# Kernel tuning notes

Hardware: AMD Instinct MI355X
Metric: run time of the kernel (lower is better)

The kernel has to match this reference:

```python
import jax, jax.numpy as jnp
import numpy as np

N = 1 << 20          # ray samples
POS_DIM = 32         # levels * feature_dim (hash_encoding is identity stub)
DENSITY_W = 64
COLOR_W = 64


def sh4_encoding(d):
    # Fourth-order (degree-4, 16-component) real spherical harmonics, vectorized.
    x, y, z = d[..., 0], d[..., 1], d[..., 2]
    xx, yy, zz = x * x, y * y, z * z
    c0 = jnp.full_like(x, 0.28209479177387814)
    comps = [
        c0,
        0.4886025119029199 * y,
        0.4886025119029199 * z,
        0.4886025119029199 * x,
        1.0925484305920792 * x * y,
        1.0925484305920792 * y * z,
        0.9461746957575601 * zz - 0.31539156525252,
        1.0925484305920792 * x * z,
        0.5462742152960396 * (xx - yy),
        0.5900435899266435 * y * (3 * xx - yy),
        2.890611442640554 * x * y * z,
        0.4570457994644658 * y * (5 * zz - 1),
        0.3731763325901154 * z * (5 * zz - 3),
        0.4570457994644658 * x * (5 * zz - 1),
        1.445305721320277 * z * (xx - yy),
        0.5900435899266435 * x * (xx - 3 * yy),
    ]
    return jnp.stack(comps, axis=-1)  # [..., 16]


def setup_inputs() -> dict:
    key = jax.random.key(0)
    ks = jax.random.split(key, 8)
    def dense_init(k, fan_in, fan_out):
        # flax default: lecun_normal kernel, zeros bias
        w = jax.random.normal(k, (fan_in, fan_out), dtype=jnp.float32) / np.sqrt(fan_in)
        b = jnp.zeros((fan_out,), dtype=jnp.float32)
        return w, b
    position = jax.random.normal(ks[0], (N, POS_DIM), dtype=jnp.float32)
    direction = jax.random.normal(ks[1], (N, 3), dtype=jnp.float32)
    W1, b1 = dense_init(ks[2], POS_DIM, DENSITY_W)
    W2, b2 = dense_init(ks[3], DENSITY_W, 16)
    W3, b3 = dense_init(ks[4], 16 + 16, COLOR_W)
    W4, b4 = dense_init(ks[5], COLOR_W, COLOR_W)
    W5, b5 = dense_init(ks[6], COLOR_W, 3)
    return {
        "position": position, "direction": direction,
        "W1": W1, "b1": b1, "W2": W2, "b2": b2,
        "W3": W3, "b3": b3, "W4": W4, "b4": b4,
        "W5": W5, "b5": b5,
    }


def reference(position, direction, W1, b1, W2, b2, W3, b3, W4, b4, W5, b5):
    # Density MLP
    h = jax.nn.relu(position @ W1 + b1)        # [N, 64]
    density = h @ W2 + b2                      # [N, 16]
    # Color MLP on concat(density_feat, SH(dir))
    enc_dir = sh4_encoding(direction)          # [N, 16]
    c = jnp.concatenate([density, enc_dir], axis=-1)  # [N, 32]
    c = jax.nn.relu(c @ W3 + b3)               # [N, 64]
    c = jax.nn.relu(c @ W4 + b4)               # [N, 64]
    c = c @ W5 + b5                            # [N, 3]
    color = jax.nn.sigmoid(c)                  # high_dynamic_range=False
    return (density, color)
```

## Files before the change

### kernel.cpp

```cpp
#include <hip/hip_runtime.h>
#include <hip/hip_bf16.h>

typedef __bf16 bf16_t;
typedef __bf16 bf16x8 __attribute__((ext_vector_type(8)));
typedef float  f32x4  __attribute__((ext_vector_type(4)));

#define TPW   8
#define WAVES 4
#define ROWS_PER_BLOCK (WAVES * TPW * 16)
#define HSTRIDE 65
#define CSTRIDE 33

__device__ __forceinline__ bf16x8 ldrow8(const float* base, size_t elem_off) {
    const float* p = base + elem_off;
    f32x4 a = *(const f32x4*)p;
    f32x4 b = *(const f32x4*)(p + 4);
    bf16x8 r;
    #pragma unroll
    for (int j = 0; j < 4; ++j) { r[j] = (bf16_t)a[j]; r[j+4] = (bf16_t)b[j]; }
    return r;
}

__global__ __launch_bounds__(256) void nerf_fused(
    const float* __restrict__ pos, const float* __restrict__ dir,
    const float* __restrict__ W1, const float* __restrict__ b1,
    const float* __restrict__ W2, const float* __restrict__ b2,
    const float* __restrict__ W3, const float* __restrict__ b3,
    const float* __restrict__ W4, const float* __restrict__ b4,
    const float* __restrict__ W5, const float* __restrict__ b5,
    float* __restrict__ outD, float* __restrict__ outC)
{
    __shared__ float hbuf[WAVES][16 * HSTRIDE];
    __shared__ float cbuf[WAVES][16 * CSTRIDE];

    const int tid  = threadIdx.x;
    const int w    = tid >> 6;
    const int lane = tid & 63;
    const int q    = lane >> 4;
    const int n    = lane & 15;

    float* hb = hbuf[w];
    float* cb = cbuf[w];

    bf16x8 w1f[4], w2f[2], w3f[4], w4f[2][4], w5f[2];
    #pragma unroll
    for (int t = 0; t < 4; ++t)
        #pragma unroll
        for (int j = 0; j < 8; ++j)
            w1f[t][j] = (bf16_t)W1[(8*q + j) * 64 + 16*t + n];
    #pragma unroll
    for (int kt = 0; kt < 2; ++kt)
        #pragma unroll
        for (int j = 0; j < 8; ++j)
            w2f[kt][j] = (bf16_t)W2[(32*kt + 8*q + j) * 16 + n];
    #pragma unroll
    for (int t = 0; t < 4; ++t)
        #pragma unroll
        for (int j = 0; j < 8; ++j)
            w3f[t][j] = (bf16_t)W3[(8*q + j) * 64 + 16*t + n];
    #pragma unroll
    for (int kt = 0; kt < 2; ++kt)
        #pragma unroll
        for (int t = 0; t < 4; ++t)
            #pragma unroll
            for (int j = 0; j < 8; ++j)
                w4f[kt][t][j] = (bf16_t)W4[(32*kt + 8*q + j) * 64 + 16*t + n];
    #pragma unroll
    for (int kt = 0; kt < 2; ++kt)
        #pragma unroll
        for (int j = 0; j < 8; ++j)
            w5f[kt][j] = (n < 3) ? (bf16_t)W5[(32*kt + 8*q + j) * 3 + n]
                                 : (bf16_t)0.0f;
    float b1f[4], b3f[4], b4f[4];
    #pragma unroll
    for (int t = 0; t < 4; ++t) {
        b1f[t] = b1[16*t + n];
        b3f[t] = b3[16*t + n];
        b4f[t] = b4[16*t + n];
    }
    const float b2f = b2[n];
    const float b5f = (n < 3) ? b5[n] : 0.0f;

    const f32x4 zero4 = {0.f, 0.f, 0.f, 0.f};

    const int waveRow0 = blockIdx.x * ROWS_PER_BLOCK + w * (TPW * 16);

    bf16x8 pfrag = ldrow8(pos, (size_t)(waveRow0 + n) * 32 + 8*q);

    for (int t = 0; t < TPW; ++t) {
        const int row0 = waveRow0 + t * 16;
        const int tn   = (t + 1 < TPW) ? t + 1 : t;
        bf16x8 pnext = ldrow8(pos, (size_t)(waveRow0 + tn*16 + n) * 32 + 8*q);

        const size_t db = (size_t)(row0 + n) * 3;
        const float dx = dir[db + 0];
        const float dy = dir[db + 1];
        const float dz = dir[db + 2];

        f32x4 acc1[4];
        #pragma unroll
        for (int tt = 0; tt < 4; ++tt)
            acc1[tt] = __builtin_amdgcn_mfma_f32_16x16x32_bf16(pfrag, w1f[tt], zero4, 0, 0, 0);
        #pragma unroll
        for (int tt = 0; tt < 4; ++tt)
            #pragma unroll
            for (int r = 0; r < 4; ++r)
                hb[(4*q + r) * HSTRIDE + 16*tt + n] = fmaxf(acc1[tt][r] + b1f[tt], 0.f);
        __syncthreads();
        bf16x8 a2[2];
        #pragma unroll
        for (int kt = 0; kt < 2; ++kt)
            #pragma unroll
            for (int j = 0; j < 8; ++j)
                a2[kt][j] = (bf16_t)hb[n * HSTRIDE + 32*kt + 8*q + j];

        f32x4 acc2 = __builtin_amdgcn_mfma_f32_16x16x32_bf16(a2[0], w2f[0], zero4, 0, 0, 0);
        acc2 = __builtin_amdgcn_mfma_f32_16x16x32_bf16(a2[1], w2f[1], acc2, 0, 0, 0);
        #pragma unroll
        for (int r = 0; r < 4; ++r)
            cb[(4*q + r) * CSTRIDE + n] = acc2[r] + b2f;

        {
            const float xx = dx*dx, yy = dy*dy, zz = dz*dz;
            float c0, c1, c2, c3;
            if (q == 0) {
                c0 = 0.28209479177387814f;
                c1 = 0.4886025119029199f * dy;
                c2 = 0.4886025119029199f * dz;
                c3 = 0.4886025119029199f * dx;
            } else if (q == 1) {
                c0 = 1.0925484305920792f * dx * dy;
                c1 = 1.0925484305920792f * dy * dz;
                c2 = 0.9461746957575601f * zz - 0.31539156525252f;
                c3 = 1.0925484305920792f * dx * dz;
            } else if (q == 2) {
                c0 = 0.5462742152960396f * (xx - yy);
                c1 = 0.5900435899266435f * dy * (3.f*xx - yy);
                c2 = 2.890611442640554f * dx * dy * dz;
                c3 = 0.4570457994644658f * dy * (5.f*zz - 1.f);
            } else {
                c0 = 0.3731763325901154f * dz * (5.f*zz - 3.f);
                c1 = 0.4570457994644658f * dx * (5.f*zz - 1.f);
                c2 = 1.445305721320277f  * dz * (xx - yy);
                c3 = 0.5900435899266435f * dx * (xx - 3.f*yy);
            }
            float* p = cb + n * CSTRIDE + 16 + 4*q;
            p[0] = c0; p[1] = c1; p[2] = c2; p[3] = c3;
        }
        __syncthreads();

        {
            const int rr = lane >> 2;
            const int cg = lane & 3;
            const float* src = cb + rr * CSTRIDE + 4*cg;
            f32x4 dv = { src[0], src[1], src[2], src[3] };
            *(f32x4*)(outD + (size_t)(row0 + rr) * 16 + 4*cg) = dv;
        }

        bf16x8 a3;
        #pragma unroll
        for (int j = 0; j < 8; ++j)
            a3[j] = (bf16_t)cb[n * CSTRIDE + 8*q + j];
        f32x4 acc3[4];
        #pragma unroll
        for (int tt = 0; tt < 4; ++tt)
            acc3[tt] = __builtin_amdgcn_mfma_f32_16x16x32_bf16(a3, w3f[tt], zero4, 0, 0, 0);
        __syncthreads();
        #pragma unroll
        for (int tt = 0; tt < 4; ++tt)
            #pragma unroll
            for (int r = 0; r < 4; ++r)
                hb[(4*q + r) * HSTRIDE + 16*tt + n] = fmaxf(acc3[tt][r] + b3f[tt], 0.f);
        __syncthreads();
        bf16x8 a4[2];
        #pragma unroll
        for (int kt = 0; kt < 2; ++kt)
            #pragma unroll
            for (int j = 0; j < 8; ++j)
                a4[kt][j] = (bf16_t)hb[n * HSTRIDE + 32*kt + 8*q + j];

        f32x4 acc4[4];
        #pragma unroll
        for (int tt = 0; tt < 4; ++tt) {
            acc4[tt] = __builtin_amdgcn_mfma_f32_16x16x32_bf16(a4[0], w4f[0][tt], zero4, 0, 0, 0);
            acc4[tt] = __builtin_amdgcn_mfma_f32_16x16x32_bf16(a4[1], w4f[1][tt], acc4[tt], 0, 0, 0);
        }
        __syncthreads();
        #pragma unroll
        for (int tt = 0; tt < 4; ++tt)
            #pragma unroll
            for (int r = 0; r < 4; ++r)
                hb[(4*q + r) * HSTRIDE + 16*tt + n] = fmaxf(acc4[tt][r] + b4f[tt], 0.f);
        __syncthreads();
        bf16x8 a5[2];
        #pragma unroll
        for (int kt = 0; kt < 2; ++kt)
            #pragma unroll
            for (int j = 0; j < 8; ++j)
                a5[kt][j] = (bf16_t)hb[n * HSTRIDE + 32*kt + 8*q + j];

        f32x4 acc5 = __builtin_amdgcn_mfma_f32_16x16x32_bf16(a5[0], w5f[0], zero4, 0, 0, 0);
        acc5 = __builtin_amdgcn_mfma_f32_16x16x32_bf16(a5[1], w5f[1], acc5, 0, 0, 0);
        if (n < 3) {
            #pragma unroll
            for (int r = 0; r < 4; ++r) {
                float v = acc5[r] + b5f;
                outC[(size_t)(row0 + 4*q + r) * 3 + n] = 1.f / (1.f + __expf(-v));
            }
        }
        __syncthreads();

        pfrag = pnext;
    }
}

extern "C" void kernel_launch(void* const* d_in, const int* in_sizes, int n_in,
                              void* d_out, int out_size, void* d_ws, size_t ws_size,
                              hipStream_t stream) {
    const float* pos = (const float*)d_in[0];
    const float* dir = (const float*)d_in[1];
    const float* W1  = (const float*)d_in[2];
    const float* b1  = (const float*)d_in[3];
    const float* W2  = (const float*)d_in[4];
    const float* b2  = (const float*)d_in[5];
    const float* W3  = (const float*)d_in[6];
    const float* b3  = (const float*)d_in[7];
    const float* W4  = (const float*)d_in[8];
    const float* b4  = (const float*)d_in[9];
    const float* W5  = (const float*)d_in[10];
    const float* b5  = (const float*)d_in[11];

    const int N = in_sizes[0] / 32;
    float* outD = (float*)d_out;
    float* outC = outD + (size_t)N * 16;

    const int grid = N / ROWS_PER_BLOCK;
    nerf_fused<<<grid, WAVES * 64, 0, stream>>>(pos, dir, W1, b1, W2, b2, W3, b3,
                                                W4, b4, W5, b5, outD, outC);
}
```

Before: 287.4 us.

## Replace block barriers with wave-local fences, vectorize LDS access, compute SH in registers

Each wave only touches its own LDS slice, so the block-wide __syncthreads calls are replaced with compiler memory fences and rely on in-wave lockstep execution. LDS strides are padded to 68/36 so rows can be read as aligned float4 vectors. The SH direction encoding is now computed straight into the MFMA A-fragment registers for the upper lane groups instead of going through LDS. Color output is staged through LDS so one store per lane replaces the strided per-lane writes. The main risk is correctness: the compiler-only fences do not emit LDS waitcnt and depend on wave-synchronous behaviour, and the padded strides may cause bank conflicts.

```diff
diff --git a/kernel.cpp b/kernel.cpp
--- a/kernel.cpp
+++ b/kernel.cpp
@@ -8,8 +8,10 @@
 #define TPW   8
 #define WAVES 4
 #define ROWS_PER_BLOCK (WAVES * TPW * 16)
-#define HSTRIDE 65
-#define CSTRIDE 33
+#define HS 68
+#define CS 36
+
+#define FENCE() __asm__ volatile("" ::: "memory")
 
 __device__ __forceinline__ bf16x8 ldrow8(const float* base, size_t elem_off) {
     const float* p = base + elem_off;
@@ -30,8 +32,8 @@
     const float* __restrict__ W5, const float* __restrict__ b5,
     float* __restrict__ outD, float* __restrict__ outC)
 {
-    __shared__ float hbuf[WAVES][16 * HSTRIDE];
-    __shared__ float cbuf[WAVES][16 * CSTRIDE];
+    __shared__ float hbuf[WAVES][16 * HS];
+    __shared__ float cbuf[WAVES][16 * CS];
 
     const int tid  = threadIdx.x;
     const int w    = tid >> 6;
@@ -92,92 +94,103 @@
         const int tn   = (t + 1 < TPW) ? t + 1 : t;
         bf16x8 pnext = ldrow8(pos, (size_t)(waveRow0 + tn*16 + n) * 32 + 8*q);
 
-        const size_t db = (size_t)(row0 + n) * 3;
-        const float dx = dir[db + 0];
-        const float dy = dir[db + 1];
-        const float dz = dir[db + 2];
-
         f32x4 acc1[4];
         #pragma unroll
         for (int tt = 0; tt < 4; ++tt)
             acc1[tt] = __builtin_amdgcn_mfma_f32_16x16x32_bf16(pfrag, w1f[tt], zero4, 0, 0, 0);
         #pragma unroll
-        for (int tt = 0; tt < 4; ++tt)
-            #pragma unroll
-            for (int r = 0; r < 4; ++r)
-                hb[(4*q + r) * HSTRIDE + 16*tt + n] = fmaxf(acc1[tt][r] + b1f[tt], 0.f);
-        __syncthreads();
+        for (int r = 0; r < 4; ++r) {
+            float* p = hb + (4*q + r) * HS + n;
+            p[0]  = fmaxf(acc1[0][r] + b1f[0], 0.f);
+            p[16] = fmaxf(acc1[1][r] + b1f[1], 0.f);
+            p[32] = fmaxf(acc1[2][r] + b1f[2], 0.f);
+            p[48] = fmaxf(acc1[3][r] + b1f[3], 0.f);
+        }
+        FENCE();
         bf16x8 a2[2];
         #pragma unroll
-        for (int kt = 0; kt < 2; ++kt)
-            #pragma unroll
-            for (int j = 0; j < 8; ++j)
-                a2[kt][j] = (bf16_t)hb[n * HSTRIDE + 32*kt + 8*q + j];
+        for (int kt = 0; kt < 2; ++kt) {
+            const f32x4* pr = (const f32x4*)(hb + n * HS + 32*kt + 8*q);
+            f32x4 u0 = pr[0], u1 = pr[1];
+            #pragma unroll
+            for (int j = 0; j < 4; ++j) { a2[kt][j] = (bf16_t)u0[j]; a2[kt][4+j] = (bf16_t)u1[j]; }
+        }
 
         f32x4 acc2 = __builtin_amdgcn_mfma_f32_16x16x32_bf16(a2[0], w2f[0], zero4, 0, 0, 0);
         acc2 = __builtin_amdgcn_mfma_f32_16x16x32_bf16(a2[1], w2f[1], acc2, 0, 0, 0);
-        #pragma unroll
-        for (int r = 0; r < 4; ++r)
-            cb[(4*q + r) * CSTRIDE + n] = acc2[r] + b2f;
-
         {
-            const float xx = dx*dx, yy = dy*dy, zz = dz*dz;
-            float c0, c1, c2, c3;
-            if (q == 0) {
-                c0 = 0.28209479177387814f;
-                c1 = 0.4886025119029199f * dy;
-                c2 = 0.4886025119029199f * dz;
-                c3 = 0.4886025119029199f * dx;
-            } else if (q == 1) {
-                c0 = 1.0925484305920792f * dx * dy;
-                c1 = 1.0925484305920792f * dy * dz;
-                c2 = 0.9461746957575601f * zz - 0.31539156525252f;
-                c3 = 1.0925484305920792f * dx * dz;
-            } else if (q == 2) {
-                c0 = 0.5462742152960396f * (xx - yy);
-                c1 = 0.5900435899266435f * dy * (3.f*xx - yy);
-                c2 = 2.890611442640554f * dx * dy * dz;
-                c3 = 0.4570457994644658f * dy * (5.f*zz - 1.f);
-            } else {
-                c0 = 0.3731763325901154f * dz * (5.f*zz - 3.f);
-                c1 = 0.4570457994644658f * dx * (5.f*zz - 1.f);
-                c2 = 1.445305721320277f  * dz * (xx - yy);
-                c3 = 0.5900435899266435f * dx * (xx - 3.f*yy);
-            }
-            float* p = cb + n * CSTRIDE + 16 + 4*q;
-            p[0] = c0; p[1] = c1; p[2] = c2; p[3] = c3;
-        }
-        __syncthreads();
+            float* p = cb + (4*q) * CS + n;
+            p[0]    = acc2[0] + b2f;
+            p[CS]   = acc2[1] + b2f;
+            p[2*CS] = acc2[2] + b2f;
+            p[3*CS] = acc2[3] + b2f;
+        }
+        FENCE();
 
         {
             const int rr = lane >> 2;
             const int cg = lane & 3;
-            const float* src = cb + rr * CSTRIDE + 4*cg;
-            f32x4 dv = { src[0], src[1], src[2], src[3] };
+            f32x4 dv = *(const f32x4*)(cb + rr * CS + 4*cg);
             *(f32x4*)(outD + (size_t)(row0 + rr) * 16 + 4*cg) = dv;
         }
 
+        float av[8];
+        {
+            const f32x4* pr = (const f32x4*)(cb + n * CS + 8*(q & 1));
+            f32x4 u0 = pr[0], u1 = pr[1];
+            #pragma unroll
+            for (int j = 0; j < 4; ++j) { av[j] = u0[j]; av[4+j] = u1[j]; }
+        }
+        if (q >= 2) {
+            const size_t db = (size_t)(row0 + n) * 3;
+            const float x = dir[db + 0], y = dir[db + 1], z = dir[db + 2];
+            const float xx = x*x, yy = y*y, zz = z*z;
+            if (q == 2) {
+                av[0] = 0.28209479177387814f;
+                av[1] = 0.4886025119029199f * y;
+                av[2] = 0.4886025119029199f * z;
+                av[3] = 0.4886025119029199f * x;
+                av[4] = 1.0925484305920792f * x * y;
+                av[5] = 1.0925484305920792f * y * z;
+                av[6] = 0.9461746957575601f * zz - 0.31539156525252f;
+                av[7] = 1.0925484305920792f * x * z;
+            } else {
+                av[0] = 0.5462742152960396f * (xx - yy);
+                av[1] = 0.5900435899266435f * y * (3.f*xx - yy);
+                av[2] = 2.890611442640554f * x * y * z;
+                av[3] = 0.4570457994644658f * y * (5.f*zz - 1.f);
+                av[4] = 0.3731763325901154f * z * (5.f*zz - 3.f);
+                av[5] = 0.4570457994644658f * x * (5.f*zz - 1.f);
+                av[6] = 1.445305721320277f  * z * (xx - yy);
+                av[7] = 0.5900435899266435f * x * (xx - 3.f*yy);
+            }
+        }
         bf16x8 a3;
         #pragma unroll
-        for (int j = 0; j < 8; ++j)
-            a3[j] = (bf16_t)cb[n * CSTRIDE + 8*q + j];
+        for (int j = 0; j < 8; ++j) a3[j] = (bf16_t)av[j];
+
         f32x4 acc3[4];
         #pragma unroll
         for (int tt = 0; tt < 4; ++tt)
             acc3[tt] = __builtin_amdgcn_mfma_f32_16x16x32_bf16(a3, w3f[tt], zero4, 0, 0, 0);
-        __syncthreads();
-        #pragma unroll
-        for (int tt = 0; tt < 4; ++tt)
-            #pragma unroll
-            for (int r = 0; r < 4; ++r)
-                hb[(4*q + r) * HSTRIDE + 16*tt + n] = fmaxf(acc3[tt][r] + b3f[tt], 0.f);
-        __syncthreads();
+        FENCE();
+        #pragma unroll
+        for (int r = 0; r < 4; ++r) {
+            float* p = hb + (4*q + r) * HS + n;
+            p[0]  = fmaxf(acc3[0][r] + b3f[0], 0.f);
+            p[16] = fmaxf(acc3[1][r] + b3f[1], 0.f);
+            p[32] = fmaxf(acc3[2][r] + b3f[2], 0.f);
+            p[48] = fmaxf(acc3[3][r] + b3f[3], 0.f);
+        }
+        FENCE();
         bf16x8 a4[2];
         #pragma unroll
-        for (int kt = 0; kt < 2; ++kt)
-            #pragma unroll
-            for (int j = 0; j < 8; ++j)
-                a4[kt][j] = (bf16_t)hb[n * HSTRIDE + 32*kt + 8*q + j];
+        for (int kt = 0; kt < 2; ++kt) {
+            const f32x4* pr = (const f32x4*)(hb + n * HS + 32*kt + 8*q);
+            f32x4 u0 = pr[0], u1 = pr[1];
+            #pragma unroll
+            for (int j = 0; j < 4; ++j) { a4[kt][j] = (bf16_t)u0[j]; a4[kt][4+j] = (bf16_t)u1[j]; }
+        }
 
         f32x4 acc4[4];
         #pragma unroll
@@ -185,30 +198,41 @@
             acc4[tt] = __builtin_amdgcn_mfma_f32_16x16x32_bf16(a4[0], w4f[0][tt], zero4, 0, 0, 0);
             acc4[tt] = __builtin_amdgcn_mfma_f32_16x16x32_bf16(a4[1], w4f[1][tt], acc4[tt], 0, 0, 0);
         }
-        __syncthreads();
-        #pragma unroll
-        for (int tt = 0; tt < 4; ++tt)
-            #pragma unroll
-            for (int r = 0; r < 4; ++r)
-                hb[(4*q + r) * HSTRIDE + 16*tt + n] = fmaxf(acc4[tt][r] + b4f[tt], 0.f);
-        __syncthreads();
+        FENCE();
+        #pragma unroll
+        for (int r = 0; r < 4; ++r) {
+            float* p = hb + (4*q + r) * HS + n;
+            p[0]  = fmaxf(acc4[0][r] + b4f[0], 0.f);
+            p[16] = fmaxf(acc4[1][r] + b4f[1], 0.f);
+            p[32] = fmaxf(acc4[2][r] + b4f[2], 0.f);
+            p[48] = fmaxf(acc4[3][r] + b4f[3], 0.f);
+        }
+        FENCE();
         bf16x8 a5[2];
         #pragma unroll
-        for (int kt = 0; kt < 2; ++kt)
-            #pragma unroll
-            for (int j = 0; j < 8; ++j)
-                a5[kt][j] = (bf16_t)hb[n * HSTRIDE + 32*kt + 8*q + j];
+        for (int kt = 0; kt < 2; ++kt) {
+            const f32x4* pr = (const f32x4*)(hb + n * HS + 32*kt + 8*q);
+            f32x4 u0 = pr[0], u1 = pr[1];
+            #pragma unroll
+            for (int j = 0; j < 4; ++j) { a5[kt][j] = (bf16_t)u0[j]; a5[kt][4+j] = (bf16_t)u1[j]; }
+        }
 
         f32x4 acc5 = __builtin_amdgcn_mfma_f32_16x16x32_bf16(a5[0], w5f[0], zero4, 0, 0, 0);
         acc5 = __builtin_amdgcn_mfma_f32_16x16x32_bf16(a5[1], w5f[1], acc5, 0, 0, 0);
         if (n < 3) {
+            float* p = cb + (4*q) * CS + 32 + n;
             #pragma unroll
             for (int r = 0; r < 4; ++r) {
                 float v = acc5[r] + b5f;
-                outC[(size_t)(row0 + 4*q + r) * 3 + n] = 1.f / (1.f + __expf(-v));
+                p[r*CS] = 1.f / (1.f + __expf(-v));
             }
         }
-        __syncthreads();
+        FENCE();
+        if (lane < 48) {
+            const int s = lane / 3, c = lane - 3*s;
+            outC[(size_t)(row0 + s) * 3 + c] = cb[s * CS + 32 + c];
+        }
+        FENCE();
 
         pfrag = pnext;
     }
```

After: 283.7 us. No clear change (-1.3%).
